# Kernel tuning notes

Measured on AMD Instinct MI355X. Metric: run time of the kernel, lower is better.

The kernel has to match this reference:

```python
import jax, jax.numpy as jnp
import numpy as np

N_NODES = 100000
N_EDGES = 1200000
D_IN = 64
D_OUT = 64


def setup_inputs() -> dict:
    key = jax.random.key(0)
    k1, k2, k3, k4, k5 = jax.random.split(key, 5)
    feat = jax.random.normal(k1, (N_NODES, D_IN), dtype=jnp.float32)
    src = jax.random.randint(k2, (N_EDGES,), 0, N_NODES, dtype=jnp.int64)
    dst = jax.random.randint(k3, (N_EDGES,), 0, N_NODES, dtype=jnp.int64)
    # xavier-uniform-ish init scaled like nn.init.xavier_uniform_ with relu gain
    gain = float(np.sqrt(2.0))
    bound = gain * float(np.sqrt(6.0 / (D_IN + D_OUT)))
    W_self = jax.random.uniform(k4, (D_OUT, D_IN), dtype=jnp.float32, minval=-bound, maxval=bound)
    W_neigh = jax.random.uniform(k5, (D_OUT, D_IN), dtype=jnp.float32, minval=-bound, maxval=bound)
    b = jnp.zeros((D_OUT,), dtype=jnp.float32)
    return {"feat": feat, "src": src, "dst": dst, "W_self": W_self, "W_neigh": W_neigh, "b": b}


def reference(feat, src, dst, W_self, W_neigh, b):
    # SAGE 'mean' aggregation: gather source features along edges, scatter-mean into dst
    msgs = feat[src]                                   # [E, D_in] gather
    agg = jax.ops.segment_sum(msgs, dst, num_segments=N_NODES)      # [N, D_in]
    deg = jax.ops.segment_sum(jnp.ones((N_EDGES,), feat.dtype), dst, num_segments=N_NODES)
    h_neigh = agg / jnp.maximum(deg, 1.0)[:, None]     # mean over in-neighbors
    # out = fc_self(feat_dst) + fc_neigh(h_neigh) + bias  (feat_drop=0 -> identity)
    out = feat @ W_self.T + h_neigh @ W_neigh.T + b
    return out
```

## Files before the change

kernel.cpp:

```cpp
#include <hip/hip_runtime.h>

#define D 64
#define NCHUNK 256
#define BSHIFT 7
#define BNODES 128
#define MAXBUK 1024
#define CAPB 1792


typedef __attribute__((ext_vector_type(8))) short bf16x8;
typedef __attribute__((ext_vector_type(4))) float f32x4;

static __device__ __forceinline__ unsigned f2bf(float f)
{
    unsigned u = __float_as_uint(f);
    unsigned r = 0x7fffu + ((u >> 16) & 1u);
    return (u + r) >> 16;
}

static __device__ __forceinline__ void cvt8(const float* __restrict__ s,
                                            unsigned short* __restrict__ d)
{
    const float4 a = *(const float4*)s;
    const float4 b = *(const float4*)(s + 4);
    uint4 p;
    p.x = f2bf(a.x) | (f2bf(a.y) << 16);
    p.y = f2bf(a.z) | (f2bf(a.w) << 16);
    p.z = f2bf(b.x) | (f2bf(b.y) << 16);
    p.w = f2bf(b.z) | (f2bf(b.w) << 16);
    *(uint4*)d = p;
}

__global__ __launch_bounds__(256) void k_prep(
    const float* __restrict__ feat, unsigned short* __restrict__ featbf,
    const float* __restrict__ Ws, const float* __restrict__ Wn,
    unsigned short* __restrict__ wsbf, unsigned short* __restrict__ wnbf,
    int* __restrict__ gcur, int n8, int nBuckets)
{
    const int t = threadIdx.x;
    if (blockIdx.x == 0)
        for (int i = t; i < nBuckets; i += 256) gcur[i] = i * CAPB;
    if (blockIdx.x == 1)
        for (int i = t; i < (D * D) / 8; i += 256) {
            cvt8(Ws + i * 8, wsbf + i * 8);
            cvt8(Wn + i * 8, wnbf + i * 8);
        }
    for (int i = blockIdx.x * 256 + t; i < n8; i += gridDim.x * 256)
        cvt8(feat + (size_t)i * 8, featbf + (size_t)i * 8);
}

__global__ __launch_bounds__(256) void k_part(
    const int* __restrict__ src, const int* __restrict__ dst,
    int* __restrict__ gcur, int* __restrict__ edata,
    int nEdges, int nBuckets, int chunk)
{
    __shared__ int cnt[MAXBUK];
    __shared__ int cur[MAXBUK];
    const int t = threadIdx.x;
    for (int i = t; i < nBuckets; i += 256) cnt[i] = 0;
    __syncthreads();
    const int beg = blockIdx.x * chunk;
    const int end = min(beg + chunk, nEdges);
    for (int i = beg + t; i < end; i += 256)
        atomicAdd(&cnt[dst[i] >> BSHIFT], 1);
    __syncthreads();
    for (int i = t; i < nBuckets; i += 256) {
        const int c = cnt[i];
        if (c) cur[i] = atomicAdd(&gcur[i], c);
    }
    __syncthreads();
    for (int i = beg + t; i < end; i += 256) {
        const int dv = dst[i];
        const int b  = dv >> BSHIFT;
        const int p  = atomicAdd(&cur[b], 1);
        edata[p] = src[i] | ((dv & (BNODES - 1)) << 20);
    }
}

__global__ __launch_bounds__(256) void k_fill3(
    const int* __restrict__ edata, const int* __restrict__ gcur,
    int2* __restrict__ rowdeg, int* __restrict__ eidx, int nNodes)
{
    __shared__ int cnt[BNODES], pos[BNODES], cur[BNODES];
    const int b = blockIdx.x, t = threadIdx.x;
    const int beg = b * CAPB;
    const int end = gcur[b];

    if (t < BNODES) cnt[t] = 0;
    __syncthreads();
    for (int i = beg + t; i < end; i += 256)
        atomicAdd(&cnt[edata[i] >> 20], 1);
    __syncthreads();
    if (t < BNODES) pos[t] = cnt[t];
    __syncthreads();
    for (int off = 1; off < BNODES; off <<= 1) {
        const int u = (t < BNODES && t >= off) ? pos[t - off] : 0;
        __syncthreads();
        if (t < BNODES) pos[t] += u;
        __syncthreads();
    }
    if (t < BNODES) {
        pos[t] -= cnt[t];
        cur[t]  = beg + pos[t];
        const int node = b * BNODES + t;
        if (node < nNodes) rowdeg[node] = make_int2(beg + pos[t], cnt[t]);
    }
    __syncthreads();
    for (int i = beg + t; i < end; i += 256) {
        const int e = edata[i];
        const int p = atomicAdd(&cur[e >> 20], 1);
        eidx[p] = (e & 0xFFFFF) << 7;
    }
}

__global__ __launch_bounds__(256) void k_agg32(
    const unsigned short* __restrict__ featbf,
    const int2* __restrict__ rowdeg,
    const int* __restrict__ eidx,
    unsigned short* __restrict__ hmeanbf, int nNodes)
{
    const int lane = threadIdx.x & 63;
    const int half = lane >> 5;
    const int ch   = lane & 31;
    const char* bp = (const char*)featbf + ch * 4;
    const int wid  = (blockIdx.x * blockDim.x + threadIdx.x) >> 6;
    const int nW   = (gridDim.x * blockDim.x) >> 6;

    int n = wid;
    if (n >= nNodes) return;
    int2 rd = rowdeg[n];
    int sv = (lane < min(rd.y, 64)) ? eidx[rd.x + lane] : 0;

    while (true) {
        const int nn = n + nW;
        int2 rdN = make_int2(0, 0);
        if (nn < nNodes) rdN = rowdeg[nn];

        const int m0 = rd.y;
        float a0 = 0.f, a1 = 0.f;
        int svN = 0;
        bool svNdone = false;

#define BATCH16(SVREG, JBASE, M)                                          \
        {                                                                 \
            int      o0, o1, o2, o3, o4, o5, o6, o7;                      \
            unsigned v0 = 0u, v1 = 0u, v2 = 0u, v3 = 0u;                  \
            unsigned v4 = 0u, v5 = 0u, v6 = 0u, v7 = 0u;                  \
            o0 = __shfl(SVREG, (JBASE) +  0 + half, 64);                  \
            o1 = __shfl(SVREG, (JBASE) +  2 + half, 64);                  \
            o2 = __shfl(SVREG, (JBASE) +  4 + half, 64);                  \
            o3 = __shfl(SVREG, (JBASE) +  6 + half, 64);                  \
            o4 = __shfl(SVREG, (JBASE) +  8 + half, 64);                  \
            o5 = __shfl(SVREG, (JBASE) + 10 + half, 64);                  \
            o6 = __shfl(SVREG, (JBASE) + 12 + half, 64);                  \
            o7 = __shfl(SVREG, (JBASE) + 14 + half, 64);                  \
            if ((JBASE) +  0 + half < (M)) v0 = *(const unsigned*)(bp + o0); \
            if ((JBASE) +  2 + half < (M)) v1 = *(const unsigned*)(bp + o1); \
            if ((JBASE) +  4 + half < (M)) v2 = *(const unsigned*)(bp + o2); \
            if ((JBASE) +  6 + half < (M)) v3 = *(const unsigned*)(bp + o3); \
            if ((JBASE) +  8 + half < (M)) v4 = *(const unsigned*)(bp + o4); \
            if ((JBASE) + 10 + half < (M)) v5 = *(const unsigned*)(bp + o5); \
            if ((JBASE) + 12 + half < (M)) v6 = *(const unsigned*)(bp + o6); \
            if ((JBASE) + 14 + half < (M)) v7 = *(const unsigned*)(bp + o7); \
            if (!svNdone) {      \
                svNdone = true;                                           \
                if (nn < nNodes && lane < min(rdN.y, 64))                 \
                    svN = eidx[rdN.x + lane];                             \
            }                                                             \
            a0 += __uint_as_float(v0 << 16);                              \
            a1 += __uint_as_float(v0 & 0xffff0000u);                      \
            a0 += __uint_as_float(v1 << 16);                              \
            a1 += __uint_as_float(v1 & 0xffff0000u);                      \
            a0 += __uint_as_float(v2 << 16);                              \
            a1 += __uint_as_float(v2 & 0xffff0000u);                      \
            a0 += __uint_as_float(v3 << 16);                              \
            a1 += __uint_as_float(v3 & 0xffff0000u);                      \
            a0 += __uint_as_float(v4 << 16);                              \
            a1 += __uint_as_float(v4 & 0xffff0000u);                      \
            a0 += __uint_as_float(v5 << 16);                              \
            a1 += __uint_as_float(v5 & 0xffff0000u);                      \
            a0 += __uint_as_float(v6 << 16);                              \
            a1 += __uint_as_float(v6 & 0xffff0000u);                      \
            a0 += __uint_as_float(v7 << 16);                              \
            a1 += __uint_as_float(v7 & 0xffff0000u);                      \
        }

        if (m0 <= 64) {
            for (int j = 0; j < m0; j += 16)
                BATCH16(sv, j, m0)
        } else {
            for (int bb = 0; bb < m0; bb += 64) {
                const int m = min(64, m0 - bb);
                const int s2 = (lane < m) ? eidx[rd.x + bb + lane] : 0;
                for (int j = 0; j < m; j += 16)
                    BATCH16(s2, j, m)
            }
        }
        if (!svNdone && nn < nNodes && lane < min(rdN.y, 64))
            svN = eidx[rdN.x + lane];
#undef BATCH16

        a0 += __shfl_xor(a0, 32, 64);
        a1 += __shfl_xor(a1, 32, 64);
        if (half == 0) {
            const float inv = 1.f / fmaxf((float)m0, 1.f);
            const unsigned p = f2bf(a0 * inv) | (f2bf(a1 * inv) << 16);
            *(unsigned*)((char*)hmeanbf + (size_t)n * (D * 2) + ch * 4) = p;
        }

        if (nn >= nNodes) break;
        n = nn; rd = rdN; sv = svN;
    }
}

__global__ __launch_bounds__(256) void k_transform_mfma(
    const unsigned short* __restrict__ featbf,
    const unsigned short* __restrict__ hmeanbf,
    const unsigned short* __restrict__ wsbf,
    const unsigned short* __restrict__ wnbf,
    const float* __restrict__ bias,
    float* __restrict__ out, int nNodes)
{
    __shared__ short Atile[64][136];
    __shared__ short Btile[64][136];

    const int t    = threadIdx.x;
    const int base = blockIdx.x * 64;

    {
        const int r = t >> 2, c = t & 3;
        const int node = base + r;
        uint4* dA = (uint4*)&Atile[r][c * 32];
        uint4* dB = (uint4*)&Btile[r][c * 32];
        const uint4* sB = (const uint4*)((c < 2) ? &wsbf[r * D + c * 32]
                                                 : &wnbf[r * D + (c - 2) * 32]);
#pragma unroll
        for (int it = 0; it < 4; ++it) dB[it] = sB[it];

        if (node < nNodes) {
            const uint4* sA = (const uint4*)((c < 2)
                ? featbf  + (size_t)node * D + c * 32
                : hmeanbf + (size_t)node * D + (c - 2) * 32);
#pragma unroll
            for (int it = 0; it < 4; ++it) dA[it] = sA[it];
        } else {
            uint4 z = {0u, 0u, 0u, 0u};
#pragma unroll
            for (int it = 0; it < 4; ++it) dA[it] = z;
        }
    }
    __syncthreads();

    const int w  = t >> 6, l = t & 63;
    const int lr = l & 15, lk = l >> 4;

    f32x4 acc[4];
#pragma unroll
    for (int cf = 0; cf < 4; ++cf) {
        const float bv = bias[cf * 16 + lr];
        acc[cf] = (f32x4){bv, bv, bv, bv};
    }
#pragma unroll
    for (int ks = 0; ks < 4; ++ks) {
        const bf16x8 av = *(const bf16x8*)&Atile[w * 16 + lr][ks * 32 + lk * 8];
#pragma unroll
        for (int cf = 0; cf < 4; ++cf) {
            const bf16x8 bv = *(const bf16x8*)&Btile[cf * 16 + lr][ks * 32 + lk * 8];
            acc[cf] = __builtin_amdgcn_mfma_f32_16x16x32_bf16(av, bv, acc[cf],
                                                              0, 0, 0);
        }
    }
#pragma unroll
    for (int cf = 0; cf < 4; ++cf) {
#pragma unroll
        for (int j = 0; j < 4; ++j) {
            const int node = base + w * 16 + lk * 4 + j;
            if (node < nNodes)
                out[(size_t)node * D + cf * 16 + lr] = acc[cf][j];
        }
    }
}

extern "C" void kernel_launch(void* const* d_in, const int* in_sizes, int n_in,
                              void* d_out, int out_size, void* d_ws, size_t ws_size,
                              hipStream_t stream)
{
    const float* feat = (const float*)d_in[0];
    const int*   src  = (const int*)  d_in[1];
    const int*   dst  = (const int*)  d_in[2];
    const float* Ws   = (const float*)d_in[3];
    const float* Wn   = (const float*)d_in[4];
    const float* bias = (const float*)d_in[5];
    float*       out  = (float*)d_out;

    const int nEdges   = in_sizes[1];
    const int nNodes   = in_sizes[0] / D;
    const int nBuckets = (nNodes + BNODES - 1) >> BSHIFT;
    const int chunk    = (nEdges + NCHUNK - 1) / NCHUNK;
    const int nBT      = (nNodes + 63) / 64;

    int*  gcur   = (int*)d_ws;
    int2* rowdeg = (int2*)(gcur + 1024);
    int*  edata  = (int*)(rowdeg + nNodes);
    int*  eidx   = edata + nBuckets * CAPB;
    unsigned short* wsbf    = (unsigned short*)(eidx + nBuckets * CAPB);
    unsigned short* wnbf    = wsbf + D * D;
    unsigned short* featbf  = wnbf + D * D;
    unsigned short* hmeanbf = featbf + (size_t)nNodes * D;

    k_prep <<<1024, 256, 0, stream>>>(feat, featbf, Ws, Wn, wsbf, wnbf,
                                      gcur, nNodes * D / 8, nBuckets);
    k_part <<<NCHUNK, 256, 0, stream>>>(src, dst, gcur, edata,
                                        nEdges, nBuckets, chunk);
    k_fill3<<<nBuckets, 256, 0, stream>>>(edata, gcur, rowdeg, eidx, nNodes);
    k_agg32<<<4096, 256, 0, stream>>>(featbf, rowdeg, eidx, hmeanbf, nNodes);
    k_transform_mfma<<<nBT, 256, 0, stream>>>(featbf, hmeanbf, wsbf, wnbf,
                                              bias, out, nNodes);
}
```

Baseline: 84.57 us.

## Fuse neighbor aggregation into MFMA transform and fold feature cast into partition

Aggregation now runs inside the MFMA transform kernel. Each wave gathers and averages neighbor features for its 16 rows and writes the bf16 mean straight into the shared A tile, so the hmean buffer is never written to or read back from global memory. The fp32-to-bf16 feature conversion moves into the edge-partition kernel, and weight conversion plus counter init go into a single-block init kernel, removing one launch. The cost is parallelism: aggregation goes from 4096 persistent blocks to one 64-node block per tile, with each wave walking 16 nodes serially, which may hide gather latency less well and leave load imbalance across waves. The partition kernel also runs on only 256 blocks, so the cast loop gets less parallelism.

```diff
diff --git a/kernel.cpp b/kernel.cpp
--- a/kernel.cpp
+++ b/kernel.cpp
@@ -31,32 +31,33 @@
     *(uint4*)d = p;
 }
 
-__global__ __launch_bounds__(256) void k_prep(
-    const float* __restrict__ feat, unsigned short* __restrict__ featbf,
+__global__ __launch_bounds__(256) void k_init(
+    int* __restrict__ gcur,
     const float* __restrict__ Ws, const float* __restrict__ Wn,
     unsigned short* __restrict__ wsbf, unsigned short* __restrict__ wnbf,
-    int* __restrict__ gcur, int n8, int nBuckets)
+    int nBuckets)
 {
     const int t = threadIdx.x;
-    if (blockIdx.x == 0)
-        for (int i = t; i < nBuckets; i += 256) gcur[i] = i * CAPB;
-    if (blockIdx.x == 1)
-        for (int i = t; i < (D * D) / 8; i += 256) {
-            cvt8(Ws + i * 8, wsbf + i * 8);
-            cvt8(Wn + i * 8, wnbf + i * 8);
-        }
-    for (int i = blockIdx.x * 256 + t; i < n8; i += gridDim.x * 256)
-        cvt8(feat + (size_t)i * 8, featbf + (size_t)i * 8);
-}
-
-__global__ __launch_bounds__(256) void k_part(
+    for (int i = t; i < nBuckets; i += 256) gcur[i] = i * CAPB;
+    for (int i = t; i < (D * D) / 8; i += 256) {
+        cvt8(Ws + i * 8, wsbf + i * 8);
+        cvt8(Wn + i * 8, wnbf + i * 8);
+    }
+}
+
+__global__ __launch_bounds__(256) void k_partc(
     const int* __restrict__ src, const int* __restrict__ dst,
     int* __restrict__ gcur, int* __restrict__ edata,
-    int nEdges, int nBuckets, int chunk)
+    const float* __restrict__ feat, unsigned short* __restrict__ featbf,
+    int n8, int nEdges, int nBuckets, int chunk)
 {
     __shared__ int cnt[MAXBUK];
     __shared__ int cur[MAXBUK];
     const int t = threadIdx.x;
+
+    for (int i = blockIdx.x * 256 + t; i < n8; i += gridDim.x * 256)
+        cvt8(feat + (size_t)i * 8, featbf + (size_t)i * 8);
+
     for (int i = t; i < nBuckets; i += 256) cnt[i] = 0;
     __syncthreads();
     const int beg = blockIdx.x * chunk;
@@ -113,109 +114,10 @@
     }
 }
 
-__global__ __launch_bounds__(256) void k_agg32(
+__global__ __launch_bounds__(256) void k_aggmm(
     const unsigned short* __restrict__ featbf,
     const int2* __restrict__ rowdeg,
     const int* __restrict__ eidx,
-    unsigned short* __restrict__ hmeanbf, int nNodes)
-{
-    const int lane = threadIdx.x & 63;
-    const int half = lane >> 5;
-    const int ch   = lane & 31;
-    const char* bp = (const char*)featbf + ch * 4;
-    const int wid  = (blockIdx.x * blockDim.x + threadIdx.x) >> 6;
-    const int nW   = (gridDim.x * blockDim.x) >> 6;
-
-    int n = wid;
-    if (n >= nNodes) return;
-    int2 rd = rowdeg[n];
-    int sv = (lane < min(rd.y, 64)) ? eidx[rd.x + lane] : 0;
-
-    while (true) {
-        const int nn = n + nW;
-        int2 rdN = make_int2(0, 0);
-        if (nn < nNodes) rdN = rowdeg[nn];
-
-        const int m0 = rd.y;
-        float a0 = 0.f, a1 = 0.f;
-        int svN = 0;
-        bool svNdone = false;
-
-#define BATCH16(SVREG, JBASE, M)                                          \
-        {                                                                 \
-            int      o0, o1, o2, o3, o4, o5, o6, o7;                      \
-            unsigned v0 = 0u, v1 = 0u, v2 = 0u, v3 = 0u;                  \
-            unsigned v4 = 0u, v5 = 0u, v6 = 0u, v7 = 0u;                  \
-            o0 = __shfl(SVREG, (JBASE) +  0 + half, 64);                  \
-            o1 = __shfl(SVREG, (JBASE) +  2 + half, 64);                  \
-            o2 = __shfl(SVREG, (JBASE) +  4 + half, 64);                  \
-            o3 = __shfl(SVREG, (JBASE) +  6 + half, 64);                  \
-            o4 = __shfl(SVREG, (JBASE) +  8 + half, 64);                  \
-            o5 = __shfl(SVREG, (JBASE) + 10 + half, 64);                  \
-            o6 = __shfl(SVREG, (JBASE) + 12 + half, 64);                  \
-            o7 = __shfl(SVREG, (JBASE) + 14 + half, 64);                  \
-            if ((JBASE) +  0 + half < (M)) v0 = *(const unsigned*)(bp + o0); \
-            if ((JBASE) +  2 + half < (M)) v1 = *(const unsigned*)(bp + o1); \
-            if ((JBASE) +  4 + half < (M)) v2 = *(const unsigned*)(bp + o2); \
-            if ((JBASE) +  6 + half < (M)) v3 = *(const unsigned*)(bp + o3); \
-            if ((JBASE) +  8 + half < (M)) v4 = *(const unsigned*)(bp + o4); \
-            if ((JBASE) + 10 + half < (M)) v5 = *(const unsigned*)(bp + o5); \
-            if ((JBASE) + 12 + half < (M)) v6 = *(const unsigned*)(bp + o6); \
-            if ((JBASE) + 14 + half < (M)) v7 = *(const unsigned*)(bp + o7); \
-            if (!svNdone) {      \
-                svNdone = true;                                           \
-                if (nn < nNodes && lane < min(rdN.y, 64))                 \
-                    svN = eidx[rdN.x + lane];                             \
-            }                                                             \
-            a0 += __uint_as_float(v0 << 16);                              \
-            a1 += __uint_as_float(v0 & 0xffff0000u);                      \
-            a0 += __uint_as_float(v1 << 16);                              \
-            a1 += __uint_as_float(v1 & 0xffff0000u);                      \
-            a0 += __uint_as_float(v2 << 16);                              \
-            a1 += __uint_as_float(v2 & 0xffff0000u);                      \
-            a0 += __uint_as_float(v3 << 16);                              \
-            a1 += __uint_as_float(v3 & 0xffff0000u);                      \
-            a0 += __uint_as_float(v4 << 16);                              \
-            a1 += __uint_as_float(v4 & 0xffff0000u);                      \
-            a0 += __uint_as_float(v5 << 16);                              \
-            a1 += __uint_as_float(v5 & 0xffff0000u);                      \
-            a0 += __uint_as_float(v6 << 16);                              \
-            a1 += __uint_as_float(v6 & 0xffff0000u);                      \
-            a0 += __uint_as_float(v7 << 16);                              \
-            a1 += __uint_as_float(v7 & 0xffff0000u);                      \
-        }
-
-        if (m0 <= 64) {
-            for (int j = 0; j < m0; j += 16)
-                BATCH16(sv, j, m0)
-        } else {
-            for (int bb = 0; bb < m0; bb += 64) {
-                const int m = min(64, m0 - bb);
-                const int s2 = (lane < m) ? eidx[rd.x + bb + lane] : 0;
-                for (int j = 0; j < m; j += 16)
-                    BATCH16(s2, j, m)
-            }
-        }
-        if (!svNdone && nn < nNodes && lane < min(rdN.y, 64))
-            svN = eidx[rdN.x + lane];
-#undef BATCH16
-
-        a0 += __shfl_xor(a0, 32, 64);
-        a1 += __shfl_xor(a1, 32, 64);
-        if (half == 0) {
-            const float inv = 1.f / fmaxf((float)m0, 1.f);
-            const unsigned p = f2bf(a0 * inv) | (f2bf(a1 * inv) << 16);
-            *(unsigned*)((char*)hmeanbf + (size_t)n * (D * 2) + ch * 4) = p;
-        }
-
-        if (nn >= nNodes) break;
-        n = nn; rd = rdN; sv = svN;
-    }
-}
-
-__global__ __launch_bounds__(256) void k_transform_mfma(
-    const unsigned short* __restrict__ featbf,
-    const unsigned short* __restrict__ hmeanbf,
     const unsigned short* __restrict__ wsbf,
     const unsigned short* __restrict__ wnbf,
     const float* __restrict__ bias,
@@ -226,6 +128,10 @@
 
     const int t    = threadIdx.x;
     const int base = blockIdx.x * 64;
+    const int lane = t & 63, w = t >> 6;
+    const int half = lane >> 5;
+    const int ch   = lane & 31;
+    const char* bp = (const char*)featbf + ch * 4;
 
     {
         const int r = t >> 2, c = t & 3;
@@ -237,10 +143,8 @@
 #pragma unroll
         for (int it = 0; it < 4; ++it) dB[it] = sB[it];
 
-        if (node < nNodes) {
-            const uint4* sA = (const uint4*)((c < 2)
-                ? featbf  + (size_t)node * D + c * 32
-                : hmeanbf + (size_t)node * D + (c - 2) * 32);
+        if (c < 2 && node < nNodes) {
+            const uint4* sA = (const uint4*)(featbf + (size_t)node * D + c * 32);
 #pragma unroll
             for (int it = 0; it < 4; ++it) dA[it] = sA[it];
         } else {
@@ -251,8 +155,99 @@
     }
     __syncthreads();
 
-    const int w  = t >> 6, l = t & 63;
-    const int lr = l & 15, lk = l >> 4;
+    {
+        int r = w * 16;
+        const int rEnd = r + 16;
+        int node = base + r;
+        if (node < nNodes) {
+            int2 rd = rowdeg[node];
+            int sv = (lane < min(rd.y, 64)) ? eidx[rd.x + lane] : 0;
+            while (true) {
+                const int rn = r + 1;
+                const int nodeN = base + rn;
+                const bool hasN = (rn < rEnd) && (nodeN < nNodes);
+                int2 rdN = make_int2(0, 0);
+                if (hasN) rdN = rowdeg[nodeN];
+
+                const int m0 = rd.y;
+                float a0 = 0.f, a1 = 0.f;
+                int svN = 0;
+                bool svNdone = false;
+
+#define BATCH16(SVREG, JBASE, M)                                          \
+                {                                                         \
+                    int      o0, o1, o2, o3, o4, o5, o6, o7;              \
+                    unsigned v0 = 0u, v1 = 0u, v2 = 0u, v3 = 0u;          \
+                    unsigned v4 = 0u, v5 = 0u, v6 = 0u, v7 = 0u;          \
+                    o0 = __shfl(SVREG, (JBASE) +  0 + half, 64);          \
+                    o1 = __shfl(SVREG, (JBASE) +  2 + half, 64);          \
+                    o2 = __shfl(SVREG, (JBASE) +  4 + half, 64);          \
+                    o3 = __shfl(SVREG, (JBASE) +  6 + half, 64);          \
+                    o4 = __shfl(SVREG, (JBASE) +  8 + half, 64);          \
+                    o5 = __shfl(SVREG, (JBASE) + 10 + half, 64);          \
+                    o6 = __shfl(SVREG, (JBASE) + 12 + half, 64);          \
+                    o7 = __shfl(SVREG, (JBASE) + 14 + half, 64);          \
+                    if ((JBASE) +  0 + half < (M)) v0 = *(const unsigned*)(bp + o0); \
+                    if ((JBASE) +  2 + half < (M)) v1 = *(const unsigned*)(bp + o1); \
+                    if ((JBASE) +  4 + half < (M)) v2 = *(const unsigned*)(bp + o2); \
+                    if ((JBASE) +  6 + half < (M)) v3 = *(const unsigned*)(bp + o3); \
+                    if ((JBASE) +  8 + half < (M)) v4 = *(const unsigned*)(bp + o4); \
+                    if ((JBASE) + 10 + half < (M)) v5 = *(const unsigned*)(bp + o5); \
+                    if ((JBASE) + 12 + half < (M)) v6 = *(const unsigned*)(bp + o6); \
+                    if ((JBASE) + 14 + half < (M)) v7 = *(const unsigned*)(bp + o7); \
+                    if (!svNdone) {                                       \
+                        svNdone = true;                                   \
+                        if (hasN && lane < min(rdN.y, 64))                \
+                            svN = eidx[rdN.x + lane];                     \
+                    }                                                     \
+                    a0 += __uint_as_float(v0 << 16);                      \
+                    a1 += __uint_as_float(v0 & 0xffff0000u);              \
+                    a0 += __uint_as_float(v1 << 16);                      \
+                    a1 += __uint_as_float(v1 & 0xffff0000u);              \
+                    a0 += __uint_as_float(v2 << 16);                      \
+                    a1 += __uint_as_float(v2 & 0xffff0000u);              \
+                    a0 += __uint_as_float(v3 << 16);                      \
+                    a1 += __uint_as_float(v3 & 0xffff0000u);              \
+                    a0 += __uint_as_float(v4 << 16);                      \
+                    a1 += __uint_as_float(v4 & 0xffff0000u);              \
+                    a0 += __uint_as_float(v5 << 16);                      \
+                    a1 += __uint_as_float(v5 & 0xffff0000u);              \
+                    a0 += __uint_as_float(v6 << 16);                      \
+                    a1 += __uint_as_float(v6 & 0xffff0000u);              \
+                    a0 += __uint_as_float(v7 << 16);                      \
+                    a1 += __uint_as_float(v7 & 0xffff0000u);              \
+                }
+
+                if (m0 <= 64) {
+                    for (int j = 0; j < m0; j += 16)
+                        BATCH16(sv, j, m0)
+                } else {
+                    for (int bb = 0; bb < m0; bb += 64) {
+                        const int m = min(64, m0 - bb);
+                        const int s2 = (lane < m) ? eidx[rd.x + bb + lane] : 0;
+                        for (int j = 0; j < m; j += 16)
+                            BATCH16(s2, j, m)
+                    }
+                }
+                if (!svNdone && hasN && lane < min(rdN.y, 64))
+                    svN = eidx[rdN.x + lane];
+#undef BATCH16
+
+                a0 += __shfl_xor(a0, 32, 64);
+                a1 += __shfl_xor(a1, 32, 64);
+                if (half == 0) {
+                    const float inv = 1.f / fmaxf((float)m0, 1.f);
+                    const unsigned p = f2bf(a0 * inv) | (f2bf(a1 * inv) << 16);
+                    *(unsigned*)((char*)&Atile[r][64] + ch * 4) = p;
+                }
+                if (!hasN) break;
+                r = rn; rd = rdN; sv = svN;
+            }
+        }
+    }
+    __syncthreads();
+
+    const int lr = lane & 15, lk = lane >> 4;
 
     f32x4 acc[4];
 #pragma unroll
@@ -303,17 +298,14 @@
     int2* rowdeg = (int2*)(gcur + 1024);
     int*  edata  = (int*)(rowdeg + nNodes);
     int*  eidx   = edata + nBuckets * CAPB;
-    unsigned short* wsbf    = (unsigned short*)(eidx + nBuckets * CAPB);
-    unsigned short* wnbf    = wsbf + D * D;
-    unsigned short* featbf  = wnbf + D * D;
-    unsigned short* hmeanbf = featbf + (size_t)nNodes * D;
-
-    k_prep <<<1024, 256, 0, stream>>>(feat, featbf, Ws, Wn, wsbf, wnbf,
-                                      gcur, nNodes * D / 8, nBuckets);
-    k_part <<<NCHUNK, 256, 0, stream>>>(src, dst, gcur, edata,
-                                        nEdges, nBuckets, chunk);
+    unsigned short* wsbf   = (unsigned short*)(eidx + nBuckets * CAPB);
+    unsigned short* wnbf   = wsbf + D * D;
+    unsigned short* featbf = wnbf + D * D;
+
+    k_init <<<1, 256, 0, stream>>>(gcur, Ws, Wn, wsbf, wnbf, nBuckets);
+    k_partc<<<NCHUNK, 256, 0, stream>>>(src, dst, gcur, edata, feat, featbf,
+                                        nNodes * D / 8, nEdges, nBuckets, chunk);
     k_fill3<<<nBuckets, 256, 0, stream>>>(edata, gcur, rowdeg, eidx, nNodes);
-    k_agg32<<<4096, 256, 0, stream>>>(featbf, rowdeg, eidx, hmeanbf, nNodes);
-    k_transform_mfma<<<nBT, 256, 0, stream>>>(featbf, hmeanbf, wsbf, wnbf,
-                                              bias, out, nNodes);
-}
+    k_aggmm<<<nBT, 256, 0, stream>>>(featbf, rowdeg, eidx, wsbf, wnbf,
+                                     bias, out, nNodes);
+}
```

Measured after the change: 99.02 us. +17.1%, slower.
